# Kernel tuning notes

Hardware: AMD Instinct MI355X
Metric: run time of the kernel (lower is better)

The kernel has to match this reference:

```python
import jax, jax.numpy as jnp
import numpy as np

B, S, H, E, K, DFF = 4, 2048, 1024, 8, 2, 4096


def setup_inputs() -> dict:
    key = jax.random.key(0)
    k0, k1, k2, k3 = jax.random.split(key, 4)
    sc = 0.02
    return {
        "x": jax.random.normal(k0, (B, S, H), jnp.float32),
        "gate_W": jax.random.normal(k1, (H, E), jnp.float32) * sc,
        "gate_b": jnp.zeros((E,), jnp.float32),
        "W1": jax.random.normal(k2, (H, DFF), jnp.float32) * sc,
        "b1": jnp.zeros((DFF,), jnp.float32),
        "W2": jax.random.normal(k3, (DFF, H), jnp.float32) * sc,
        "b2": jnp.zeros((H,), jnp.float32),
    }


def reference(x, gate_W, gate_b, W1, b1, W2, b2):
    b, s, h = x.shape
    x_flat = x.reshape(-1, h)                      # [T, H]
    gate_scores = x_flat @ gate_W + gate_b         # [T, E]
    top_k_scores, top_k_idx = jax.lax.top_k(gate_scores, K)   # [T, K]
    top_k_w = jax.nn.softmax(top_k_scores, axis=-1)           # [T, K]

    # All experts share the same weights (ModuleList reuses one module), so
    # sum_i w_i * expert_i(x) == expert(x) * sum_i w_i. top_k indices are
    # unique per token, so the per-token combine weight is sum of top-k weights.
    hdd = jax.nn.gelu(x_flat @ W1 + b1, approximate=False)    # [T, DFF]
    y = hdd @ W2 + b2                                         # [T, H]
    tok_w = top_k_w.sum(axis=-1)                              # [T] (== 1.0)
    output = (y * tok_w[:, None]).reshape(b, s, h)

    expert_load = gate_scores.mean(axis=0)                    # [E]
    aux_loss = (expert_load ** 2).sum()
    exp_counts = jnp.zeros((E,), jnp.int32).at[top_k_idx.ravel()].add(1)
    return output, aux_loss, exp_counts
```

## Files before the change

kernel.cpp:

```cpp
#include <hip/hip_runtime.h>
#include <hip/hip_bf16.h>
#include <math.h>

#define Tn   8192
#define Hn   1024
#define En   8
#define DFFn 4096

typedef __attribute__((ext_vector_type(8))) short bf16x8;
typedef __attribute__((ext_vector_type(8))) unsigned short u16x8;
typedef __attribute__((ext_vector_type(4))) float f32x4;

static __device__ inline unsigned short f2bf(float f) {
    __hip_bfloat16 h = __float2bfloat16(f);
    return __builtin_bit_cast(unsigned short, h);
}

__global__ __launch_bounds__(256) void prep(
    const float* __restrict__ W1, unsigned short* __restrict__ W1t,
    const float* __restrict__ W2, unsigned short* __restrict__ W2t,
    const float* __restrict__ x, const float* __restrict__ gW,
    const float* __restrict__ gb, unsigned short* __restrict__ xbf,
    float* __restrict__ tokw, float* __restrict__ load_sum,
    int* __restrict__ counts)
{
    __shared__ float smem[8 * 1024 + En];
    __shared__ int   s_cnt[En];
    const int tid = threadIdx.x;
    const int id  = blockIdx.x;

    if (id < 512) {
        const float* src; unsigned short* dst; int SR, SC, tb;
        if (id < 256) { src = W1; dst = W1t; SR = Hn;   SC = DFFn; tb = id; }
        else          { src = W2; dst = W2t; SR = DFFn; SC = Hn;   tb = id - 256; }
        const int tcs = SC >> 7;
        const int tr  = tb / tcs, tc = tb - tr * tcs;
        const int r0  = tr << 7, c0 = tc << 7;
        unsigned short* tile = (unsigned short*)smem;

        #pragma unroll
        for (int i = 0; i < 16; ++i) {
            int idx = tid + i * 256;
            int r = idx >> 5, c4 = (idx & 31) << 2;
            float4 v = *(const float4*)(src + (size_t)(r0 + r) * SC + c0 + c4);
            int cs = c4 ^ (((r >> 3) & 7) << 2);
            ushort4 pk;
            pk.x = f2bf(v.x); pk.y = f2bf(v.y);
            pk.z = f2bf(v.z); pk.w = f2bf(v.w);
            *(ushort4*)(tile + r * 128 + cs) = pk;
        }
        __syncthreads();
        #pragma unroll
        for (int i = 0; i < 8; ++i) {
            int idx = tid + i * 256;
            int n = idx >> 4, kg = idx & 15, k0 = kg << 3;
            int s = (kg & 7) << 2;
            u16x8 o;
            #pragma unroll
            for (int j = 0; j < 8; ++j)
                o[j] = tile[(k0 + j) * 128 + (n ^ s)];
            *(u16x8*)(dst + (size_t)(c0 + n) * SR + r0 + k0) = o;
        }
        return;
    }

    const int gid = id - 512;
    float* gwt    = smem;
    float* s_load = smem + 8 * 1024;
    if (tid < En) { s_load[tid] = 0.f; s_cnt[tid] = 0; }
    #pragma unroll
    for (int i = 0; i < 32; ++i) {
        int f = tid + i * 256;
        gwt[(f & 7) * 1024 + (f >> 3)] = gW[f];
    }
    __syncthreads();

    const int lane = tid & 63;
    const int wv   = tid >> 6;

    for (int tok = gid * 4 + wv; tok < Tn; tok += 4096) {
        const float4* xr = (const float4*)(x + (size_t)tok * Hn);
        float acc[8] = {0.f,0.f,0.f,0.f,0.f,0.f,0.f,0.f};
        #pragma unroll
        for (int j = 0; j < Hn / 256; ++j) {
            int h4 = j * 64 + lane;
            float4 xv = xr[h4];
            ushort4 pk;
            pk.x = f2bf(xv.x); pk.y = f2bf(xv.y);
            pk.z = f2bf(xv.z); pk.w = f2bf(xv.w);
            ((ushort4*)xbf)[(size_t)tok * (Hn / 4) + h4] = pk;
            #pragma unroll
            for (int e = 0; e < 8; ++e) {
                const float4 w = *(const float4*)(gwt + e * 1024 + h4 * 4);
                acc[e] += xv.x * w.x + xv.y * w.y + xv.z * w.z + xv.w * w.w;
            }
        }
        #pragma unroll
        for (int e = 0; e < 8; ++e) {
            float v = acc[e];
            #pragma unroll
            for (int off = 32; off > 0; off >>= 1) v += __shfl_xor(v, off, 64);
            acc[e] = v + gb[e];
        }
        if (lane == 0) {
            #pragma unroll
            for (int e = 0; e < 8; ++e) atomicAdd(&s_load[e], acc[e]);
            int i1 = 0; float v1 = acc[0];
            #pragma unroll
            for (int e = 1; e < 8; ++e) if (acc[e] > v1) { v1 = acc[e]; i1 = e; }
            int i2 = -1; float v2 = -3.0e38f;
            #pragma unroll
            for (int e = 0; e < 8; ++e) if (e != i1 && acc[e] > v2) { v2 = acc[e]; i2 = e; }
            atomicAdd(&s_cnt[i1], 1);
            atomicAdd(&s_cnt[i2], 1);
            float e2 = __expf(v2 - v1);
            float t  = 1.0f + e2;
            tokw[tok] = 1.0f / t + e2 / t;
        }
    }
    __syncthreads();
    if (tid < En) {
        atomicAdd(&load_sum[tid], s_load[tid]);
        atomicAdd(&counts[tid],   s_cnt[tid]);
    }
}

static __device__ inline bf16x8 ldsfrag(const char* base, int row, int chunk) {
    return *(const bf16x8*)(base + row * 128 + (((chunk) ^ (row & 7)) << 4));
}

template<int BN, int WM, int WN, int EPI, int TPB>
__global__ __launch_bounds__(512, 2) void gemm8(
    const __hip_bfloat16* __restrict__ A,
    const __hip_bfloat16* __restrict__ Bt,
    const float* __restrict__ bias,
    const float* __restrict__ tokw,
    void* __restrict__ C, int N, int K, int nx,
    const float* __restrict__ load_sum, const int* __restrict__ counts,
    float* __restrict__ out_tail, int nblk)
{
    constexpr int BM = 256;
    constexpr int MR = (BM / WM) / 16;
    constexpr int NR = (BN / WN) / 16;
    constexpr int AU = BM / 64;
    constexpr int BU = BN / 64;
    constexpr int ABYTES = BM * 64 * 2;
    constexpr int BBYTES = BN * 64 * 2;
    constexpr int TILEB  = ABYTES + BBYTES;

    extern __shared__ char lds[];

    const int tid = threadIdx.x;
    const int id  = blockIdx.x;

    if (EPI == 0 && id >= nblk) {
        if (tid == 0) {
            float aux = 0.f;
            #pragma unroll
            for (int e = 0; e < En; ++e) {
                float m = load_sum[e] * (1.0f / (float)Tn);
                aux += m * m;
            }
            out_tail[0] = aux;
            #pragma unroll
            for (int e = 0; e < En; ++e) out_tail[1 + e] = (float)counts[e];
        }
        return;
    }

    const int lane = tid & 63;
    const int wid  = tid >> 6;
    const int wn   = wid % WN;
    const int wm   = wid / WN;
    const int wrow = wm * (BM / WM);
    const int wcol = wn * (BN / WN);
    const int fr   = lane & 15;
    const int fq   = lane >> 4;

    const int sr = tid >> 3;
    const int sc = (tid & 7) ^ (sr & 7);

    int m0, n0;
    unsigned aOff[AU], bOff[BU];
    auto setup = [&](int t) {
        int g   = id + t * nblk;
        int xcd = g & 7;
        int wg  = xcd * ((nblk * TPB) >> 3) + (g >> 3);
        int by  = wg / nx, bx = wg - by * nx;
        m0 = by * BM; n0 = bx * BN;
        #pragma unroll
        for (int u = 0; u < AU; ++u)
            aOff[u] = (unsigned)((m0 + u * 64 + sr) * K + sc * 8);
        #pragma unroll
        for (int u = 0; u < BU; ++u)
            bOff[u] = (unsigned)((n0 + u * 64 + sr) * K + sc * 8);
    };
    setup(0);

#define STA(b, u, kt) __builtin_amdgcn_global_load_lds( \
    (const __attribute__((address_space(1))) void*)(A + aOff[u] + (unsigned)(kt) * 64u), \
    (__attribute__((address_space(3))) void*)(lds + (b) * TILEB + (u) * 8192 + tid * 16), 16, 0, 0)
#define STB(b, u, kt) __builtin_amdgcn_global_load_lds( \
    (const __attribute__((address_space(1))) void*)(Bt + bOff[u] + (unsigned)(kt) * 64u), \
    (__attribute__((address_space(3))) void*)(lds + (b) * TILEB + ABYTES + (u) * 8192 + tid * 16), 16, 0, 0)

#define PROLOG_G0 do { \
    STA(0,0,0); STA(0,1,0); STA(0,2,0); STA(0,3,0); \
    STB(0,0,0); STB(0,1,0); STB(0,2,0); STB(0,3,0); \
    STA(1,0,1); STA(1,2,1); \
    STB(1,0,1); STB(1,1,1); STB(1,2,1); STB(1,3,1); } while (0)

    bf16x8 af[MR / 2][2];
    bf16x8 bfr[4][2];
    f32x4  acc[MR][NR];
    const f32x4 zero = {0.f, 0.f, 0.f, 0.f};
    #pragma unroll
    for (int i = 0; i < MR; ++i)
        #pragma unroll
        for (int j = 0; j < NR; ++j) acc[i][j] = zero;

#define RDA(b, half) do { _Pragma("unroll") \
    for (int m_ = 0; m_ < MR / 2; ++m_) { _Pragma("unroll") \
        for (int ks_ = 0; ks_ < 2; ++ks_) \
            af[m_][ks_] = ldsfrag(lds + (b) * TILEB, \
                wrow + ((half) * (MR / 2) + m_) * 16 + fr, ks_ * 4 + fq); } } while (0)

#define RDB(b, half) do { _Pragma("unroll") \
    for (int n_ = 0; n_ < 2; ++n_) { _Pragma("unroll") \
        for (int ks_ = 0; ks_ < 2; ++ks_) \
            bfr[(half) * 2 + n_][ks_] = ldsfrag(lds + (b) * TILEB + ABYTES, \
                wcol + ((half) * 2 + n_) * 16 + fr, ks_ * 4 + fq); } } while (0)

#define MFMAQ(hm, hn) do { \
    __builtin_amdgcn_s_setprio(1); \
    _Pragma("unroll") \
    for (int m_ = 0; m_ < MR / 2; ++m_) { _Pragma("unroll") \
        for (int n_ = 0; n_ < 2; ++n_) { _Pragma("unroll") \
            for (int ks_ = 0; ks_ < 2; ++ks_) \
                acc[(hm) * (MR / 2) + m_][(hn) * 2 + n_] = \
                    __builtin_amdgcn_mfma_f32_16x16x32_bf16( \
                        af[m_][ks_], bfr[(hn) * 2 + n_][ks_], \
                        acc[(hm) * (MR / 2) + m_][(hn) * 2 + n_], 0, 0, 0); } } \
    __builtin_amdgcn_s_setprio(0); } while (0)

#define MFMAQ1(hm) do { \
    __builtin_amdgcn_s_setprio(1); \
    _Pragma("unroll") \
    for (int m_ = 0; m_ < MR / 2; ++m_) { _Pragma("unroll") \
        for (int n_ = 0; n_ < NR; ++n_) { _Pragma("unroll") \
            for (int ks_ = 0; ks_ < 2; ++ks_) \
                acc[(hm) * (MR / 2) + m_][n_] = \
                    __builtin_amdgcn_mfma_f32_16x16x32_bf16( \
                        bfr[n_][ks_], af[m_][ks_], \
                        acc[(hm) * (MR / 2) + m_][n_], 0, 0, 0); } } \
    __builtin_amdgcn_s_setprio(0); } while (0)

#define MIDSYNC do { \
    __builtin_amdgcn_sched_barrier(0); \
    __builtin_amdgcn_s_barrier(); \
    asm volatile("s_waitcnt lgkmcnt(0)" ::: "memory"); \
    __builtin_amdgcn_sched_barrier(0); } while (0)

#define ENDBAR do { \
    __builtin_amdgcn_sched_barrier(0); \
    __builtin_amdgcn_s_barrier(); \
    __builtin_amdgcn_sched_barrier(0); } while (0)

#define DRAIN6 do { asm volatile("s_waitcnt vmcnt(6)" ::: "memory"); \
    __builtin_amdgcn_sched_barrier(0); } while (0)
#define DRAIN2 do { asm volatile("s_waitcnt vmcnt(2)" ::: "memory"); \
    __builtin_amdgcn_sched_barrier(0); } while (0)

    const int KT = K >> 6;

    if constexpr (WM == 2) {
        PROLOG_G0;
        DRAIN6;
        __builtin_amdgcn_s_barrier();
        __builtin_amdgcn_sched_barrier(0);

        for (int tt = 0; tt < TPB; ++tt) {
            for (int i = 0; i < (KT >> 1); ++i) {
                const int t1 = 2 * i + 1;
                const int c2 = (2 * i + 2 < KT) ? 2 * i + 2 : KT - 1;
                const int c3 = (2 * i + 3 < KT) ? 2 * i + 3 : KT - 1;

                RDA(0, 0); RDB(0, 0);
                STA(1,1,t1); STA(1,3,t1);
                MIDSYNC; MFMAQ(0, 0); ENDBAR;
                RDB(0, 1);
                STA(0,0,c2); STA(0,2,c2);
                MIDSYNC; MFMAQ(0, 1); ENDBAR;
                RDA(0, 1);
                STB(0,0,c2); STB(0,1,c2);
                MIDSYNC; MFMAQ(1, 0); ENDBAR;
                STB(0,2,c2); STB(0,3,c2);
                MIDSYNC; MFMAQ(1, 1); DRAIN6; ENDBAR;
                RDA(1, 0); RDB(1, 0);
                STA(0,1,c2); STA(0,3,c2);
                MIDSYNC; MFMAQ(0, 0); ENDBAR;
                RDB(1, 1);
                STA(1,0,c3); STA(1,2,c3);
                MIDSYNC; MFMAQ(0, 1); ENDBAR;
                RDA(1, 1);
                STB(1,0,c3); STB(1,1,c3);
                MIDSYNC; MFMAQ(1, 0); ENDBAR;
                STB(1,2,c3); STB(1,3,c3);
                MIDSYNC; MFMAQ(1, 1); DRAIN6; ENDBAR;
            }

            const int em0 = m0, en0 = n0;
            if (tt + 1 < TPB) {
                asm volatile("s_waitcnt vmcnt(0)" ::: "memory");
                __builtin_amdgcn_sched_barrier(0);
            }
            float bias4[NR];
            #pragma unroll
            for (int ni = 0; ni < NR; ++ni)
                bias4[ni] = bias[en0 + wcol + ni * 16 + fr];
            if (tt + 1 < TPB) {
                setup(tt + 1);
                PROLOG_G0;
            }
            #pragma unroll
            for (int mi = 0; mi < MR; ++mi) {
                #pragma unroll
                for (int ni = 0; ni < NR; ++ni) {
                    const int col = en0 + wcol + ni * 16 + fr;
                    const int rb  = em0 + wrow + mi * 16 + fq * 4;
                    #pragma unroll
                    for (int i2 = 0; i2 < 4; ++i2) {
                        float u  = acc[mi][ni][i2] + bias4[ni];
                        float uu = u * u;
                        float z  = u * __fmaf_rn(uu, -0.07135607f, -1.59576912f);
                        float e  = __expf(z);
                        float g  = u * __builtin_amdgcn_rcpf(1.0f + e);
                        ((__hip_bfloat16*)C)[(size_t)(rb + i2) * N + col] =
                            __float2bfloat16(g);
                    }
                }
            }
            if (tt + 1 < TPB) {
                #pragma unroll
                for (int i = 0; i < MR; ++i)
                    #pragma unroll
                    for (int j = 0; j < NR; ++j) acc[i][j] = zero;
                asm volatile("s_waitcnt vmcnt(38)" ::: "memory");
                __builtin_amdgcn_sched_barrier(0);
                __builtin_amdgcn_s_barrier();
                __builtin_amdgcn_sched_barrier(0);
            }
        }
    } else {
        STA(0,0,0); STA(0,1,0); STA(0,2,0); STA(0,3,0);
        STB(0,0,0); STB(0,1,0);
        STB(1,0,1); STB(1,1,1);
        DRAIN2;
        __builtin_amdgcn_s_barrier();
        __builtin_amdgcn_sched_barrier(0);

        for (int i = 0; i < (KT >> 1); ++i) {
            const int t1 = 2 * i + 1;
            const int c2 = (2 * i + 2 < KT) ? 2 * i + 2 : KT - 1;
            const int c3 = (2 * i + 3 < KT) ? 2 * i + 3 : KT - 1;

            RDA(0, 0); RDB(0, 0); RDB(0, 1);
            STA(1,0,t1); STA(1,1,t1); STA(1,2,t1); STA(1,3,t1);
            MIDSYNC; MFMAQ1(0); ENDBAR;
            RDA(0, 1);
            STB(0,0,c2); STB(0,1,c2);
            MIDSYNC; MFMAQ1(1); DRAIN2; ENDBAR;
            RDA(1, 0); RDB(1, 0); RDB(1, 1);
            STA(0,0,c2); STA(0,1,c2); STA(0,2,c2); STA(0,3,c2);
            MIDSYNC; MFMAQ1(0); ENDBAR;
            RDA(1, 1);
            STB(1,0,c3); STB(1,1,c3);
            MIDSYNC; MFMAQ1(1); DRAIN2; ENDBAR;
        }

        const int mrow0 = m0 + wrow + fr;
        const int ncol0 = n0 + wcol + fq * 4;
        float4 b4[NR];
        #pragma unroll
        for (int ni = 0; ni < NR; ++ni)
            b4[ni] = *(const float4*)(bias + ncol0 + ni * 16);

        #pragma unroll
        for (int mi = 0; mi < MR; ++mi) {
            const int row = mrow0 + mi * 16;
            const float tw = tokw[row];
            #pragma unroll
            for (int ni = 0; ni < NR; ++ni) {
                f32x4 v = acc[mi][ni];
                float4 o;
                o.x = (v[0] + b4[ni].x) * tw;
                o.y = (v[1] + b4[ni].y) * tw;
                o.z = (v[2] + b4[ni].z) * tw;
                o.w = (v[3] + b4[ni].w) * tw;
                *(float4*)((float*)C + (size_t)row * N + ncol0 + ni * 16) = o;
            }
        }
    }

#undef STA
#undef STB
#undef PROLOG_G0
#undef RDA
#undef RDB
#undef MFMAQ
#undef MFMAQ1
#undef MIDSYNC
#undef ENDBAR
#undef DRAIN6
#undef DRAIN2
}

extern "C" void kernel_launch(void* const* d_in, const int* in_sizes, int n_in,
                              void* d_out, int out_size, void* d_ws, size_t ws_size,
                              hipStream_t stream)
{
    const float* x  = (const float*)d_in[0];
    const float* gW = (const float*)d_in[1];
    const float* gb = (const float*)d_in[2];
    const float* W1 = (const float*)d_in[3];
    const float* b1 = (const float*)d_in[4];
    const float* W2 = (const float*)d_in[5];
    const float* b2 = (const float*)d_in[6];
    float* out = (float*)d_out;

    char* ws = (char*)d_ws;
    __hip_bfloat16* xbf = (__hip_bfloat16*)ws;  ws += (size_t)Tn * Hn * 2;
    __hip_bfloat16* W1t = (__hip_bfloat16*)ws;  ws += (size_t)Hn * DFFn * 2;
    __hip_bfloat16* W2t = (__hip_bfloat16*)ws;  ws += (size_t)Hn * DFFn * 2;
    __hip_bfloat16* hdd = (__hip_bfloat16*)ws;  ws += (size_t)Tn * DFFn * 2;
    float* tokw     = (float*)ws;               ws += (size_t)Tn * 4;
    float* load_sum = (float*)ws;               ws += En * 4;
    int*   counts   = (int*)ws;                 ws += En * 4;

    static bool attr_done = false;
    if (!attr_done) {
        (void)hipFuncSetAttribute(
            reinterpret_cast<const void*>(&gemm8<256, 2, 4, 0, 2>),
            hipFuncAttributeMaxDynamicSharedMemorySize, 131072);
        (void)hipFuncSetAttribute(
            reinterpret_cast<const void*>(&gemm8<128, 4, 2, 1, 1>),
            hipFuncAttributeMaxDynamicSharedMemorySize, 98304);
        attr_done = true;
    }

    hipMemsetAsync(load_sum, 0, En * 4 * 2, stream);

    prep<<<1536, 256, 0, stream>>>(W1, (unsigned short*)W1t,
                                   W2, (unsigned short*)W2t,
                                   x, gW, gb, (unsigned short*)xbf,
                                   tokw, load_sum, counts);

    gemm8<256, 2, 4, 0, 2><<<257, 512, 131072, stream>>>(
        xbf, W1t, b1, nullptr, hdd, DFFn, Hn, 16,
        load_sum, counts, out + (size_t)Tn * Hn, 256);

    gemm8<128, 4, 2, 1, 1><<<256, 512, 98304, stream>>>(
        hdd, W2t, b2, tokw, out, Hn, DFFn, 8,
        nullptr, nullptr, nullptr, 256);
}
```

Baseline: 284.7 us.

## Replace persistent two-tile GEMM1 with one tile per block and finer LDS waits

The first GEMM stops being persistent: instead of each of 256 blocks processing two output tiles with an overlapped epilogue/prologue, it launches 512 blocks with one tile each. Both GEMM kernels also split their LDS fragment reads and MFMA groups into smaller pieces with incremental lgkmcnt waits, so MFMAs can start as soon as their operands arrive rather than after a full lgkmcnt(0) drain. This is meant to hide LDS read latency behind MFMA work. In exchange, GEMM1 loses the overlap of one tile's epilogue with the next tile's loads and pays per-block launch and prologue cost twice as often.

```diff
diff --git a/kernel.cpp b/kernel.cpp
--- a/kernel.cpp
+++ b/kernel.cpp
@@ -129,7 +129,7 @@
     return *(const bf16x8*)(base + row * 128 + (((chunk) ^ (row & 7)) << 4));
 }
 
-template<int BN, int WM, int WN, int EPI, int TPB>
+template<int BN, int WM, int WN, int EPI>
 __global__ __launch_bounds__(512, 2) void gemm8(
     const __hip_bfloat16* __restrict__ A,
     const __hip_bfloat16* __restrict__ Bt,
@@ -168,6 +168,11 @@
         return;
     }
 
+    int wg = id;
+    { int xcd = wg & 7, idx = wg >> 3; wg = xcd * (nblk >> 3) + idx; }
+    const int by = wg / nx, bx = wg % nx;
+    const int m0 = by * BM, n0 = bx * BN;
+
     const int lane = tid & 63;
     const int wid  = tid >> 6;
     const int wn   = wid % WN;
@@ -179,23 +184,13 @@
 
     const int sr = tid >> 3;
     const int sc = (tid & 7) ^ (sr & 7);
-
-    int m0, n0;
     unsigned aOff[AU], bOff[BU];
-    auto setup = [&](int t) {
-        int g   = id + t * nblk;
-        int xcd = g & 7;
-        int wg  = xcd * ((nblk * TPB) >> 3) + (g >> 3);
-        int by  = wg / nx, bx = wg - by * nx;
-        m0 = by * BM; n0 = bx * BN;
-        #pragma unroll
-        for (int u = 0; u < AU; ++u)
-            aOff[u] = (unsigned)((m0 + u * 64 + sr) * K + sc * 8);
-        #pragma unroll
-        for (int u = 0; u < BU; ++u)
-            bOff[u] = (unsigned)((n0 + u * 64 + sr) * K + sc * 8);
-    };
-    setup(0);
+    #pragma unroll
+    for (int u = 0; u < AU; ++u)
+        aOff[u] = (unsigned)((m0 + u * 64 + sr) * K + sc * 8);
+    #pragma unroll
+    for (int u = 0; u < BU; ++u)
+        bOff[u] = (unsigned)((n0 + u * 64 + sr) * K + sc * 8);
 
 #define STA(b, u, kt) __builtin_amdgcn_global_load_lds( \
     (const __attribute__((address_space(1))) void*)(A + aOff[u] + (unsigned)(kt) * 64u), \
@@ -204,12 +199,6 @@
     (const __attribute__((address_space(1))) void*)(Bt + bOff[u] + (unsigned)(kt) * 64u), \
     (__attribute__((address_space(3))) void*)(lds + (b) * TILEB + ABYTES + (u) * 8192 + tid * 16), 16, 0, 0)
 
-#define PROLOG_G0 do { \
-    STA(0,0,0); STA(0,1,0); STA(0,2,0); STA(0,3,0); \
-    STB(0,0,0); STB(0,1,0); STB(0,2,0); STB(0,3,0); \
-    STA(1,0,1); STA(1,2,1); \
-    STB(1,0,1); STB(1,1,1); STB(1,2,1); STB(1,3,1); } while (0)
-
     bf16x8 af[MR / 2][2];
     bf16x8 bfr[4][2];
     f32x4  acc[MR][NR];
@@ -219,53 +208,54 @@
         #pragma unroll
         for (int j = 0; j < NR; ++j) acc[i][j] = zero;
 
-#define RDA(b, half) do { _Pragma("unroll") \
+#define RD_A1(b, half, m_) do { _Pragma("unroll") \
+    for (int ks_ = 0; ks_ < 2; ++ks_) \
+        af[m_][ks_] = ldsfrag(lds + (b) * TILEB, \
+            wrow + ((half) * (MR / 2) + (m_)) * 16 + fr, ks_ * 4 + fq); } while (0)
+#define RD_B1(b, nn) do { _Pragma("unroll") \
+    for (int ks_ = 0; ks_ < 2; ++ks_) \
+        bfr[nn][ks_] = ldsfrag(lds + (b) * TILEB + ABYTES, \
+            wcol + (nn) * 16 + fr, ks_ * 4 + fq); } while (0)
+
+#define MFMA_M(hm, hn, m_) do { _Pragma("unroll") \
+    for (int n_ = 0; n_ < 2; ++n_) { _Pragma("unroll") \
+        for (int ks_ = 0; ks_ < 2; ++ks_) \
+            acc[(hm) * (MR / 2) + (m_)][(hn) * 2 + n_] = \
+                __builtin_amdgcn_mfma_f32_16x16x32_bf16( \
+                    af[m_][ks_], bfr[(hn) * 2 + n_][ks_], \
+                    acc[(hm) * (MR / 2) + (m_)][(hn) * 2 + n_], 0, 0, 0); } } while (0)
+#define MFMA_N(hm, nn) do { _Pragma("unroll") \
     for (int m_ = 0; m_ < MR / 2; ++m_) { _Pragma("unroll") \
         for (int ks_ = 0; ks_ < 2; ++ks_) \
-            af[m_][ks_] = ldsfrag(lds + (b) * TILEB, \
-                wrow + ((half) * (MR / 2) + m_) * 16 + fr, ks_ * 4 + fq); } } while (0)
-
-#define RDB(b, half) do { _Pragma("unroll") \
-    for (int n_ = 0; n_ < 2; ++n_) { _Pragma("unroll") \
+            acc[(hm) * (MR / 2) + m_][nn] = \
+                __builtin_amdgcn_mfma_f32_16x16x32_bf16( \
+                    af[m_][ks_], bfr[nn][ks_], \
+                    acc[(hm) * (MR / 2) + m_][nn], 0, 0, 0); } } while (0)
+
+#define MFMA1_N(hm, nn) do { _Pragma("unroll") \
+    for (int m_ = 0; m_ < MR / 2; ++m_) { _Pragma("unroll") \
         for (int ks_ = 0; ks_ < 2; ++ks_) \
-            bfr[(half) * 2 + n_][ks_] = ldsfrag(lds + (b) * TILEB + ABYTES, \
-                wcol + ((half) * 2 + n_) * 16 + fr, ks_ * 4 + fq); } } while (0)
-
-#define MFMAQ(hm, hn) do { \
-    __builtin_amdgcn_s_setprio(1); \
-    _Pragma("unroll") \
-    for (int m_ = 0; m_ < MR / 2; ++m_) { _Pragma("unroll") \
-        for (int n_ = 0; n_ < 2; ++n_) { _Pragma("unroll") \
-            for (int ks_ = 0; ks_ < 2; ++ks_) \
-                acc[(hm) * (MR / 2) + m_][(hn) * 2 + n_] = \
-                    __builtin_amdgcn_mfma_f32_16x16x32_bf16( \
-                        af[m_][ks_], bfr[(hn) * 2 + n_][ks_], \
-                        acc[(hm) * (MR / 2) + m_][(hn) * 2 + n_], 0, 0, 0); } } \
-    __builtin_amdgcn_s_setprio(0); } while (0)
-
-#define MFMAQ1(hm) do { \
-    __builtin_amdgcn_s_setprio(1); \
-    _Pragma("unroll") \
-    for (int m_ = 0; m_ < MR / 2; ++m_) { _Pragma("unroll") \
-        for (int n_ = 0; n_ < NR; ++n_) { _Pragma("unroll") \
-            for (int ks_ = 0; ks_ < 2; ++ks_) \
-                acc[(hm) * (MR / 2) + m_][n_] = \
-                    __builtin_amdgcn_mfma_f32_16x16x32_bf16( \
-                        bfr[n_][ks_], af[m_][ks_], \
-                        acc[(hm) * (MR / 2) + m_][n_], 0, 0, 0); } } \
-    __builtin_amdgcn_s_setprio(0); } while (0)
-
-#define MIDSYNC do { \
-    __builtin_amdgcn_sched_barrier(0); \
-    __builtin_amdgcn_s_barrier(); \
-    asm volatile("s_waitcnt lgkmcnt(0)" ::: "memory"); \
-    __builtin_amdgcn_sched_barrier(0); } while (0)
-
-#define ENDBAR do { \
+            acc[(hm) * (MR / 2) + m_][nn] = \
+                __builtin_amdgcn_mfma_f32_16x16x32_bf16( \
+                    bfr[nn][ks_], af[m_][ks_], \
+                    acc[(hm) * (MR / 2) + m_][nn], 0, 0, 0); } } while (0)
+#define MFMA1_M(hm, m_) do { _Pragma("unroll") \
+    for (int n_ = 0; n_ < NR; ++n_) { _Pragma("unroll") \
+        for (int ks_ = 0; ks_ < 2; ++ks_) \
+            acc[(hm) * (MR / 2) + (m_)][n_] = \
+                __builtin_amdgcn_mfma_f32_16x16x32_bf16( \
+                    bfr[n_][ks_], af[m_][ks_], \
+                    acc[(hm) * (MR / 2) + (m_)][n_], 0, 0, 0); } } while (0)
+
+#define SBAR do { \
     __builtin_amdgcn_sched_barrier(0); \
     __builtin_amdgcn_s_barrier(); \
     __builtin_amdgcn_sched_barrier(0); } while (0)
-
+#define WAITL(n) do { \
+    asm volatile("s_waitcnt lgkmcnt(" #n ")" ::: "memory"); \
+    __builtin_amdgcn_sched_barrier(0); } while (0)
+#define PRIO1 __builtin_amdgcn_s_setprio(1)
+#define PRIO0 __builtin_amdgcn_s_setprio(0)
 #define DRAIN6 do { asm volatile("s_waitcnt vmcnt(6)" ::: "memory"); \
     __builtin_amdgcn_sched_barrier(0); } while (0)
 #define DRAIN2 do { asm volatile("s_waitcnt vmcnt(2)" ::: "memory"); \
@@ -274,81 +264,95 @@
     const int KT = K >> 6;
 
     if constexpr (WM == 2) {
-        PROLOG_G0;
+        STA(0,0,0); STA(0,1,0); STA(0,2,0); STA(0,3,0);
+        STB(0,0,0); STB(0,1,0); STB(0,2,0); STB(0,3,0);
+        STA(1,0,1); STA(1,2,1);
+        STB(1,0,1); STB(1,1,1); STB(1,2,1); STB(1,3,1);
         DRAIN6;
         __builtin_amdgcn_s_barrier();
         __builtin_amdgcn_sched_barrier(0);
 
-        for (int tt = 0; tt < TPB; ++tt) {
-            for (int i = 0; i < (KT >> 1); ++i) {
-                const int t1 = 2 * i + 1;
-                const int c2 = (2 * i + 2 < KT) ? 2 * i + 2 : KT - 1;
-                const int c3 = (2 * i + 3 < KT) ? 2 * i + 3 : KT - 1;
-
-                RDA(0, 0); RDB(0, 0);
-                STA(1,1,t1); STA(1,3,t1);
-                MIDSYNC; MFMAQ(0, 0); ENDBAR;
-                RDB(0, 1);
-                STA(0,0,c2); STA(0,2,c2);
-                MIDSYNC; MFMAQ(0, 1); ENDBAR;
-                RDA(0, 1);
-                STB(0,0,c2); STB(0,1,c2);
-                MIDSYNC; MFMAQ(1, 0); ENDBAR;
-                STB(0,2,c2); STB(0,3,c2);
-                MIDSYNC; MFMAQ(1, 1); DRAIN6; ENDBAR;
-                RDA(1, 0); RDB(1, 0);
-                STA(0,1,c2); STA(0,3,c2);
-                MIDSYNC; MFMAQ(0, 0); ENDBAR;
-                RDB(1, 1);
-                STA(1,0,c3); STA(1,2,c3);
-                MIDSYNC; MFMAQ(0, 1); ENDBAR;
-                RDA(1, 1);
-                STB(1,0,c3); STB(1,1,c3);
-                MIDSYNC; MFMAQ(1, 0); ENDBAR;
-                STB(1,2,c3); STB(1,3,c3);
-                MIDSYNC; MFMAQ(1, 1); DRAIN6; ENDBAR;
-            }
-
-            const int em0 = m0, en0 = n0;
-            if (tt + 1 < TPB) {
-                asm volatile("s_waitcnt vmcnt(0)" ::: "memory");
-                __builtin_amdgcn_sched_barrier(0);
-            }
-            float bias4[NR];
-            #pragma unroll
-            for (int ni = 0; ni < NR; ++ni)
-                bias4[ni] = bias[en0 + wcol + ni * 16 + fr];
-            if (tt + 1 < TPB) {
-                setup(tt + 1);
-                PROLOG_G0;
-            }
-            #pragma unroll
-            for (int mi = 0; mi < MR; ++mi) {
+        for (int i = 0; i < (KT >> 1); ++i) {
+            const int t1 = 2 * i + 1;
+            const int c2 = (2 * i + 2 < KT) ? 2 * i + 2 : KT - 1;
+            const int c3 = (2 * i + 3 < KT) ? 2 * i + 3 : KT - 1;
+
+            RD_B1(0,0); RD_B1(0,1);
+            RD_A1(0,0,0); RD_A1(0,0,1); RD_A1(0,0,2); RD_A1(0,0,3);
+            STA(1,1,t1); STA(1,3,t1);
+            SBAR; PRIO1;
+            WAITL(6); MFMA_M(0,0,0);
+            WAITL(4); MFMA_M(0,0,1);
+            WAITL(2); MFMA_M(0,0,2);
+            WAITL(0); MFMA_M(0,0,3);
+            PRIO0; SBAR;
+            RD_B1(0,2); RD_B1(0,3);
+            STA(0,0,c2); STA(0,2,c2);
+            SBAR; PRIO1;
+            WAITL(2); MFMA_N(0,2);
+            WAITL(0); MFMA_N(0,3);
+            PRIO0; SBAR;
+            RD_A1(0,1,0); RD_A1(0,1,1); RD_A1(0,1,2); RD_A1(0,1,3);
+            STB(0,0,c2); STB(0,1,c2);
+            SBAR; PRIO1;
+            WAITL(6); MFMA_M(1,0,0);
+            WAITL(4); MFMA_M(1,0,1);
+            WAITL(2); MFMA_M(1,0,2);
+            WAITL(0); MFMA_M(1,0,3);
+            PRIO0; SBAR;
+            STB(0,2,c2); STB(0,3,c2);
+            SBAR; PRIO1;
+            MFMA_M(1,1,0); MFMA_M(1,1,1); MFMA_M(1,1,2); MFMA_M(1,1,3);
+            PRIO0; DRAIN6; SBAR;
+            RD_B1(1,0); RD_B1(1,1);
+            RD_A1(1,0,0); RD_A1(1,0,1); RD_A1(1,0,2); RD_A1(1,0,3);
+            STA(0,1,c2); STA(0,3,c2);
+            SBAR; PRIO1;
+            WAITL(6); MFMA_M(0,0,0);
+            WAITL(4); MFMA_M(0,0,1);
+            WAITL(2); MFMA_M(0,0,2);
+            WAITL(0); MFMA_M(0,0,3);
+            PRIO0; SBAR;
+            RD_B1(1,2); RD_B1(1,3);
+            STA(1,0,c3); STA(1,2,c3);
+            SBAR; PRIO1;
+            WAITL(2); MFMA_N(0,2);
+            WAITL(0); MFMA_N(0,3);
+            PRIO0; SBAR;
+            RD_A1(1,1,0); RD_A1(1,1,1); RD_A1(1,1,2); RD_A1(1,1,3);
+            STB(1,0,c3); STB(1,1,c3);
+            SBAR; PRIO1;
+            WAITL(6); MFMA_M(1,0,0);
+            WAITL(4); MFMA_M(1,0,1);
+            WAITL(2); MFMA_M(1,0,2);
+            WAITL(0); MFMA_M(1,0,3);
+            PRIO0; SBAR;
+            STB(1,2,c3); STB(1,3,c3);
+            SBAR; PRIO1;
+            MFMA_M(1,1,0); MFMA_M(1,1,1); MFMA_M(1,1,2); MFMA_M(1,1,3);
+            PRIO0; DRAIN6; SBAR;
+        }
+
+        float bias4[NR];
+        #pragma unroll
+        for (int ni = 0; ni < NR; ++ni)
+            bias4[ni] = bias[n0 + wcol + ni * 16 + fr];
+        #pragma unroll
+        for (int mi = 0; mi < MR; ++mi) {
+            #pragma unroll
+            for (int ni = 0; ni < NR; ++ni) {
+                const int col = n0 + wcol + ni * 16 + fr;
+                const int rb  = m0 + wrow + mi * 16 + fq * 4;
                 #pragma unroll
-                for (int ni = 0; ni < NR; ++ni) {
-                    const int col = en0 + wcol + ni * 16 + fr;
-                    const int rb  = em0 + wrow + mi * 16 + fq * 4;
-                    #pragma unroll
-                    for (int i2 = 0; i2 < 4; ++i2) {
-                        float u  = acc[mi][ni][i2] + bias4[ni];
-                        float uu = u * u;
-                        float z  = u * __fmaf_rn(uu, -0.07135607f, -1.59576912f);
-                        float e  = __expf(z);
-                        float g  = u * __builtin_amdgcn_rcpf(1.0f + e);
-                        ((__hip_bfloat16*)C)[(size_t)(rb + i2) * N + col] =
-                            __float2bfloat16(g);
-                    }
+                for (int i2 = 0; i2 < 4; ++i2) {
+                    float u  = acc[mi][ni][i2] + bias4[ni];
+                    float uu = u * u;
+                    float z  = u * __fmaf_rn(uu, -0.07135607f, -1.59576912f);
+                    float e  = __expf(z);
+                    float g  = u * __builtin_amdgcn_rcpf(1.0f + e);
+                    ((__hip_bfloat16*)C)[(size_t)(rb + i2) * N + col] =
+                        __float2bfloat16(g);
                 }
-            }
-            if (tt + 1 < TPB) {
-                #pragma unroll
-                for (int i = 0; i < MR; ++i)
-                    #pragma unroll
-                    for (int j = 0; j < NR; ++j) acc[i][j] = zero;
-                asm volatile("s_waitcnt vmcnt(38)" ::: "memory");
-                __builtin_amdgcn_sched_barrier(0);
-                __builtin_amdgcn_s_barrier();
-                __builtin_amdgcn_sched_barrier(0);
             }
         }
     } else {
@@ -364,18 +368,36 @@
             const int c2 = (2 * i + 2 < KT) ? 2 * i + 2 : KT - 1;
             const int c3 = (2 * i + 3 < KT) ? 2 * i + 3 : KT - 1;
 
-            RDA(0, 0); RDB(0, 0); RDB(0, 1);
+            RD_A1(0,0,0); RD_A1(0,0,1);
+            RD_B1(0,0); RD_B1(0,1); RD_B1(0,2); RD_B1(0,3);
             STA(1,0,t1); STA(1,1,t1); STA(1,2,t1); STA(1,3,t1);
-            MIDSYNC; MFMAQ1(0); ENDBAR;
-            RDA(0, 1);
+            SBAR; PRIO1;
+            WAITL(6); MFMA1_N(0,0);
+            WAITL(4); MFMA1_N(0,1);
+            WAITL(2); MFMA1_N(0,2);
+            WAITL(0); MFMA1_N(0,3);
+            PRIO0; SBAR;
+            RD_A1(0,1,0); RD_A1(0,1,1);
             STB(0,0,c2); STB(0,1,c2);
-            MIDSYNC; MFMAQ1(1); DRAIN2; ENDBAR;
-            RDA(1, 0); RDB(1, 0); RDB(1, 1);
+            SBAR; PRIO1;
+            WAITL(2); MFMA1_M(1,0);
+            WAITL(0); MFMA1_M(1,1);
+            PRIO0; DRAIN2; SBAR;
+            RD_A1(1,0,0); RD_A1(1,0,1);
+            RD_B1(1,0); RD_B1(1,1); RD_B1(1,2); RD_B1(1,3);
             STA(0,0,c2); STA(0,1,c2); STA(0,2,c2); STA(0,3,c2);
-            MIDSYNC; MFMAQ1(0); ENDBAR;
-            RDA(1, 1);
+            SBAR; PRIO1;
+            WAITL(6); MFMA1_N(0,0);
+            WAITL(4); MFMA1_N(0,1);
+            WAITL(2); MFMA1_N(0,2);
+            WAITL(0); MFMA1_N(0,3);
+            PRIO0; SBAR;
+            RD_A1(1,1,0); RD_A1(1,1,1);
             STB(1,0,c3); STB(1,1,c3);
-            MIDSYNC; MFMAQ1(1); DRAIN2; ENDBAR;
+            SBAR; PRIO1;
+            WAITL(2); MFMA1_M(1,0);
+            WAITL(0); MFMA1_M(1,1);
+            PRIO0; DRAIN2; SBAR;
         }
 
         const int mrow0 = m0 + wrow + fr;
@@ -404,13 +426,16 @@
 
 #undef STA
 #undef STB
-#undef PROLOG_G0
-#undef RDA
-#undef RDB
-#undef MFMAQ
-#undef MFMAQ1
-#undef MIDSYNC
-#undef ENDBAR
+#undef RD_A1
+#undef RD_B1
+#undef MFMA_M
+#undef MFMA_N
+#undef MFMA1_N
+#undef MFMA1_M
+#undef SBAR
+#undef WAITL
+#undef PRIO1
+#undef PRIO0
 #undef DRAIN6
 #undef DRAIN2
 }
@@ -440,10 +465,10 @@
     static bool attr_done = false;
     if (!attr_done) {
         (void)hipFuncSetAttribute(
-            reinterpret_cast<const void*>(&gemm8<256, 2, 4, 0, 2>),
+            reinterpret_cast<const void*>(&gemm8<256, 2, 4, 0>),
             hipFuncAttributeMaxDynamicSharedMemorySize, 131072);
         (void)hipFuncSetAttribute(
-            reinterpret_cast<const void*>(&gemm8<128, 4, 2, 1, 1>),
+            reinterpret_cast<const void*>(&gemm8<128, 4, 2, 1>),
             hipFuncAttributeMaxDynamicSharedMemorySize, 98304);
         attr_done = true;
     }
@@ -455,11 +480,11 @@
                                    x, gW, gb, (unsigned short*)xbf,
                                    tokw, load_sum, counts);
 
-    gemm8<256, 2, 4, 0, 2><<<257, 512, 131072, stream>>>(
+    gemm8<256, 2, 4, 0><<<513, 512, 131072, stream>>>(
         xbf, W1t, b1, nullptr, hdd, DFFn, Hn, 16,
-        load_sum, counts, out + (size_t)Tn * Hn, 256);
-
-    gemm8<128, 4, 2, 1, 1><<<256, 512, 98304, stream>>>(
+        load_sum, counts, out + (size_t)Tn * Hn, 512);
+
+    gemm8<128, 4, 2, 1><<<256, 512, 98304, stream>>>(
         hdd, W2t, b2, tokw, out, Hn, DFFn, 8,
         nullptr, nullptr, nullptr, 256);
 }
```

New measurement: 267.7 us. 1.06x faster.
